# Kernel optimization log

Measured on AMD Instinct MI355X. Metric: run time of the kernel, lower is better.

The kernel has to match this reference:

```python
import jax, jax.numpy as jnp
import numpy as np

B, C, H, W = 8, 256, 64, 64


def setup_inputs() -> dict:
    key = jax.random.key(0)
    ks = jax.random.split(key, 9)
    s = 1.0 / np.sqrt(C)  # conv2d default init scale
    return {
        "foreground": jax.random.normal(ks[0], (B, C, H, W), jnp.float32),
        "background": jax.random.normal(ks[1], (B, C, H, W), jnp.float32),
        "mask": jax.random.uniform(ks[2], (B, C, H, W), jnp.float32),
        "Wq": jax.random.normal(ks[3], (C, C), jnp.float32) * s,
        "bq": jnp.zeros((C,), jnp.float32),
        "Wk": jax.random.normal(ks[4], (C, C), jnp.float32) * s,
        "bk": jnp.zeros((C,), jnp.float32),
        "Wv": jax.random.normal(ks[5], (C, C), jnp.float32) * s,
        "bv": jnp.zeros((C,), jnp.float32),
        "gamma": jnp.ones((1,), jnp.float32),
    }


def _conv1x1(x, Wt, b):
    # 1x1 conv == per-pixel channel matmul; x: [B,C,H,W], Wt: [Cout,Cin]
    return jnp.einsum('bchw,oc->bohw', x, Wt) + b[None, :, None, None]


def reference(foreground, background, mask, Wq, bq, Wk, bk, Wv, bv, gamma):
    b, c, h, w = foreground.shape
    hw = h * w
    # mask is already at feature resolution (interpolate would be identity)
    q = _conv1x1(foreground, Wq, bq).reshape(b, c, hw)   # [B,C,HW]
    k = _conv1x1(background, Wk, bk).reshape(b, c, hw)   # [B,C,HW]
    # bmm(q, k^T): channel-channel correlation [B,C,C]
    corr = jnp.einsum('bci,bdi->bcd', q, k)
    m_r = mask.reshape(b, c, hw)                          # [B,C,HW]
    # bmm(corr, m_r): mask-modulated scores [B,C,HW]
    scores = jnp.einsum('bcd,bdi->bci', corr, m_r)
    energy = jax.nn.softmax(scores, axis=-1)
    v = _conv1x1(foreground, Wv, bv).reshape(b, c, hw)
    attended = (energy * v).reshape(b, c, h, w)
    out = foreground * mask + gamma[0] * (1.0 - mask) * attended
    return out
```

## Files before the change

### kernel.cpp

```cpp
#include <hip/hip_runtime.h>
#include <math.h>

#define B_    8
#define C_    256
#define HW_   4096
#define CHW_  ((long)C_ * HW_)

#define BKT   32
#define LDH   40
#define KS    16
#define KCH   (HW_ / KS)

typedef __attribute__((ext_vector_type(8))) short bf16x8;
typedef __attribute__((ext_vector_type(4))) float f32x4;
#define MFMA_BF16(a, b, c) __builtin_amdgcn_mfma_f32_16x16x32_bf16((a), (b), (c), 0, 0, 0)

__device__ __forceinline__ void cvt_hl4(const float4 f, uint* h, uint* l) {
    uint u0 = __float_as_uint(f.x), u1 = __float_as_uint(f.y),
         u2 = __float_as_uint(f.z), u3 = __float_as_uint(f.w);
    uint h0 = (u0 + 0x8000u) & 0xFFFF0000u, h1 = (u1 + 0x8000u) & 0xFFFF0000u,
         h2 = (u2 + 0x8000u) & 0xFFFF0000u, h3 = (u3 + 0x8000u) & 0xFFFF0000u;
    h[0] = (h0 >> 16) | h1;
    h[1] = (h2 >> 16) | h3;
    float l0 = f.x - __uint_as_float(h0), l1 = f.y - __uint_as_float(h1),
          l2 = f.z - __uint_as_float(h2), l3 = f.w - __uint_as_float(h3);
    uint a0 = __float_as_uint(l0) & 0xFFFF0000u, a1 = __float_as_uint(l1) & 0xFFFF0000u,
         a2 = __float_as_uint(l2) & 0xFFFF0000u, a3 = __float_as_uint(l3) & 0xFFFF0000u;
    l[0] = (a0 >> 16) | a1;
    l[1] = (a2 >> 16) | a3;
}
__device__ __forceinline__ void cvt_h4(const float4 f, uint* h) {
    uint u0 = __float_as_uint(f.x), u1 = __float_as_uint(f.y),
         u2 = __float_as_uint(f.z), u3 = __float_as_uint(f.w);
    uint h0 = (u0 + 0x8000u) & 0xFFFF0000u, h1 = (u1 + 0x8000u) & 0xFFFF0000u,
         h2 = (u2 + 0x8000u) & 0xFFFF0000u, h3 = (u3 + 0x8000u) & 0xFFFF0000u;
    h[0] = (h0 >> 16) | h1;
    h[1] = (h2 >> 16) | h3;
}

__global__ __launch_bounds__(256, 2) void gemm_nt_mfma(
    const float* __restrict__ F, const float* __restrict__ G,
    float* __restrict__ part)
{
    __shared__ ushort Ah[128 * LDH], Al[128 * LDH], Bh[128 * LDH], Bl[128 * LDH];

    const int z  = blockIdx.z;
    const int b  = z >> 4;
    const int ks = z & (KS - 1);
    const int c0 = blockIdx.y * 128;
    const int d0 = blockIdx.x * 128;
    const float* Fb = F + (long)b * CHW_ + (long)ks * KCH;
    const float* Gb = G + (long)b * CHW_ + (long)ks * KCH;

    const int t    = threadIdx.x;
    const int srow = t >> 1;
    const int sk   = (t & 1) * 16;
    const int lane = t & 63, w = t >> 6;
    const int col  = lane & 15, quad = lane >> 4;
    const int wm   = (w >> 1) * 64, wn = (w & 1) * 64;

    f32x4 acc[4][4] = {};

    for (int kt = 0; kt < KCH; kt += BKT) {
        {
            const float* s = &Fb[(long)(c0 + srow) * HW_ + kt + sk];
            uint h[4], l[4];
            cvt_hl4(*reinterpret_cast<const float4*>(s),     h + 0, l + 0);
            cvt_hl4(*reinterpret_cast<const float4*>(s + 4), h + 2, l + 2);
            *reinterpret_cast<uint4*>(&Ah[srow * LDH + sk]) = make_uint4(h[0], h[1], h[2], h[3]);
            *reinterpret_cast<uint4*>(&Al[srow * LDH + sk]) = make_uint4(l[0], l[1], l[2], l[3]);
            cvt_hl4(*reinterpret_cast<const float4*>(s + 8),  h + 0, l + 0);
            cvt_hl4(*reinterpret_cast<const float4*>(s + 12), h + 2, l + 2);
            *reinterpret_cast<uint4*>(&Ah[srow * LDH + sk + 8]) = make_uint4(h[0], h[1], h[2], h[3]);
            *reinterpret_cast<uint4*>(&Al[srow * LDH + sk + 8]) = make_uint4(l[0], l[1], l[2], l[3]);
        }
        {
            const float* s = &Gb[(long)(d0 + srow) * HW_ + kt + sk];
            uint h[4], l[4];
            cvt_hl4(*reinterpret_cast<const float4*>(s),     h + 0, l + 0);
            cvt_hl4(*reinterpret_cast<const float4*>(s + 4), h + 2, l + 2);
            *reinterpret_cast<uint4*>(&Bh[srow * LDH + sk]) = make_uint4(h[0], h[1], h[2], h[3]);
            *reinterpret_cast<uint4*>(&Bl[srow * LDH + sk]) = make_uint4(l[0], l[1], l[2], l[3]);
            cvt_hl4(*reinterpret_cast<const float4*>(s + 8),  h + 0, l + 0);
            cvt_hl4(*reinterpret_cast<const float4*>(s + 12), h + 2, l + 2);
            *reinterpret_cast<uint4*>(&Bh[srow * LDH + sk + 8]) = make_uint4(h[0], h[1], h[2], h[3]);
            *reinterpret_cast<uint4*>(&Bl[srow * LDH + sk + 8]) = make_uint4(l[0], l[1], l[2], l[3]);
        }
        __syncthreads();

        bf16x8 bfh[4], bfl[4];
        #pragma unroll
        for (int tj = 0; tj < 4; ++tj) {
            const int r = (wn + tj * 16 + col) * LDH + quad * 8;
            bfh[tj] = *reinterpret_cast<const bf16x8*>(&Bh[r]);
            bfl[tj] = *reinterpret_cast<const bf16x8*>(&Bl[r]);
        }
        #pragma unroll
        for (int ti = 0; ti < 4; ++ti) {
            const int r = (wm + ti * 16 + col) * LDH + quad * 8;
            bf16x8 afh = *reinterpret_cast<const bf16x8*>(&Ah[r]);
            bf16x8 afl = *reinterpret_cast<const bf16x8*>(&Al[r]);
            #pragma unroll
            for (int tj = 0; tj < 4; ++tj) {
                acc[ti][tj] = MFMA_BF16(afh, bfh[tj], acc[ti][tj]);
                acc[ti][tj] = MFMA_BF16(afh, bfl[tj], acc[ti][tj]);
                acc[ti][tj] = MFMA_BF16(afl, bfh[tj], acc[ti][tj]);
            }
        }
        __syncthreads();
    }

    float* P = part + (long)z * C_ * C_;
    #pragma unroll
    for (int ti = 0; ti < 4; ++ti) {
        const int m = c0 + wm + ti * 16 + quad * 4;
        #pragma unroll
        for (int tj = 0; tj < 4; ++tj) {
            const int n = d0 + wn + tj * 16 + col;
            #pragma unroll
            for (int r = 0; r < 4; ++r)
                P[(long)(m + r) * C_ + n] = acc[ti][tj][r];
        }
    }
}

__global__ __launch_bounds__(256, 2) void gemm_scores_mfma(
    const float* __restrict__ corr,
    const ushort* __restrict__ mTh, const ushort* __restrict__ mTl,
    float* __restrict__ S)
{
    __shared__ ushort Ah[128 * LDH], Al[128 * LDH], Bh[128 * LDH], Bl[128 * LDH];

    const int b  = blockIdx.z;
    const int m0 = blockIdx.y * 128;
    const int n0 = blockIdx.x * 128;
    const float*  Ab  = corr + (long)b * C_ * C_;
    const ushort* Bhb = mTh + (long)b * CHW_;
    const ushort* Blb = mTl + (long)b * CHW_;

    const int t    = threadIdx.x;
    const int srow = t >> 1;
    const int sk   = (t & 1) * 16;
    const int lane = t & 63, w = t >> 6;
    const int col  = lane & 15, quad = lane >> 4;
    const int wm   = (w >> 1) * 64, wn = (w & 1) * 64;

    f32x4 acc[4][4] = {};

    for (int kt = 0; kt < C_; kt += BKT) {
        {
            const float* s = &Ab[(long)(m0 + srow) * C_ + kt + sk];
            uint h[4], l[4];
            cvt_hl4(*reinterpret_cast<const float4*>(s),     h + 0, l + 0);
            cvt_hl4(*reinterpret_cast<const float4*>(s + 4), h + 2, l + 2);
            *reinterpret_cast<uint4*>(&Ah[srow * LDH + sk]) = make_uint4(h[0], h[1], h[2], h[3]);
            *reinterpret_cast<uint4*>(&Al[srow * LDH + sk]) = make_uint4(l[0], l[1], l[2], l[3]);
            cvt_hl4(*reinterpret_cast<const float4*>(s + 8),  h + 0, l + 0);
            cvt_hl4(*reinterpret_cast<const float4*>(s + 12), h + 2, l + 2);
            *reinterpret_cast<uint4*>(&Ah[srow * LDH + sk + 8]) = make_uint4(h[0], h[1], h[2], h[3]);
            *reinterpret_cast<uint4*>(&Al[srow * LDH + sk + 8]) = make_uint4(l[0], l[1], l[2], l[3]);
        }
        {
            const long o = (long)(n0 + srow) * C_ + kt + sk;
            uint4 v0 = *reinterpret_cast<const uint4*>(&Bhb[o]);
            uint4 v1 = *reinterpret_cast<const uint4*>(&Bhb[o + 8]);
            uint4 w0 = *reinterpret_cast<const uint4*>(&Blb[o]);
            uint4 w1 = *reinterpret_cast<const uint4*>(&Blb[o + 8]);
            *reinterpret_cast<uint4*>(&Bh[srow * LDH + sk])     = v0;
            *reinterpret_cast<uint4*>(&Bh[srow * LDH + sk + 8]) = v1;
            *reinterpret_cast<uint4*>(&Bl[srow * LDH + sk])     = w0;
            *reinterpret_cast<uint4*>(&Bl[srow * LDH + sk + 8]) = w1;
        }
        __syncthreads();

        bf16x8 bfh[4], bfl[4];
        #pragma unroll
        for (int tj = 0; tj < 4; ++tj) {
            const int r = (wn + tj * 16 + col) * LDH + quad * 8;
            bfh[tj] = *reinterpret_cast<const bf16x8*>(&Bh[r]);
            bfl[tj] = *reinterpret_cast<const bf16x8*>(&Bl[r]);
        }
        #pragma unroll
        for (int ti = 0; ti < 4; ++ti) {
            const int r = (wm + ti * 16 + col) * LDH + quad * 8;
            bf16x8 afh = *reinterpret_cast<const bf16x8*>(&Ah[r]);
            bf16x8 afl = *reinterpret_cast<const bf16x8*>(&Al[r]);
            #pragma unroll
            for (int tj = 0; tj < 4; ++tj) {
                acc[ti][tj] = MFMA_BF16(afh, bfh[tj], acc[ti][tj]);
                acc[ti][tj] = MFMA_BF16(afh, bfl[tj], acc[ti][tj]);
                acc[ti][tj] = MFMA_BF16(afl, bfh[tj], acc[ti][tj]);
            }
        }
        __syncthreads();
    }

    float* Sb = S + (long)b * CHW_;
    #pragma unroll
    for (int ti = 0; ti < 4; ++ti) {
        const int m = m0 + wm + ti * 16 + quad * 4;
        #pragma unroll
        for (int tj = 0; tj < 4; ++tj) {
            const int n = n0 + wn + tj * 16 + col;
            #pragma unroll
            for (int r = 0; r < 4; ++r)
                Sb[(long)(m + r) * HW_ + n] = acc[ti][tj][r];
        }
    }
}

__global__ __launch_bounds__(256, 2) void gemm_v_final_mfma(
    const float* __restrict__ Wv, const ushort* __restrict__ fTh,
    const float* __restrict__ bv, const float* __restrict__ fg,
    const float* __restrict__ mask, const float* __restrict__ S,
    const float* __restrict__ stats, const float* __restrict__ gamma,
    float* __restrict__ out)
{
    __shared__ ushort Ahh[128 * LDH], Bhh[128 * LDH];

    const int b  = blockIdx.z;
    const int m0 = blockIdx.y * 128;
    const int n0 = blockIdx.x * 128;
    const ushort* Bb = fTh + (long)b * CHW_;

    const int t    = threadIdx.x;
    const int srow = t >> 1;
    const int sk   = (t & 1) * 16;
    const int lane = t & 63, w = t >> 6;
    const int col  = lane & 15, quad = lane >> 4;
    const int wm   = (w >> 1) * 64, wn = (w & 1) * 64;

    f32x4 acc[4][4] = {};

    for (int kt = 0; kt < C_; kt += BKT) {
        {
            const float* s = &Wv[(long)(m0 + srow) * C_ + kt + sk];
            uint h[4];
            cvt_h4(*reinterpret_cast<const float4*>(s),     h + 0);
            cvt_h4(*reinterpret_cast<const float4*>(s + 4), h + 2);
            *reinterpret_cast<uint4*>(&Ahh[srow * LDH + sk]) = make_uint4(h[0], h[1], h[2], h[3]);
            cvt_h4(*reinterpret_cast<const float4*>(s + 8),  h + 0);
            cvt_h4(*reinterpret_cast<const float4*>(s + 12), h + 2);
            *reinterpret_cast<uint4*>(&Ahh[srow * LDH + sk + 8]) = make_uint4(h[0], h[1], h[2], h[3]);
        }
        {
            const long o = (long)(n0 + srow) * C_ + kt + sk;
            uint4 v0 = *reinterpret_cast<const uint4*>(&Bb[o]);
            uint4 v1 = *reinterpret_cast<const uint4*>(&Bb[o + 8]);
            *reinterpret_cast<uint4*>(&Bhh[srow * LDH + sk])     = v0;
            *reinterpret_cast<uint4*>(&Bhh[srow * LDH + sk + 8]) = v1;
        }
        __syncthreads();

        bf16x8 bfh[4];
        #pragma unroll
        for (int tj = 0; tj < 4; ++tj)
            bfh[tj] = *reinterpret_cast<const bf16x8*>(&Bhh[(wn + tj * 16 + col) * LDH + quad * 8]);
        #pragma unroll
        for (int ti = 0; ti < 4; ++ti) {
            bf16x8 afh = *reinterpret_cast<const bf16x8*>(&Ahh[(wm + ti * 16 + col) * LDH + quad * 8]);
            #pragma unroll
            for (int tj = 0; tj < 4; ++tj)
                acc[ti][tj] = MFMA_BF16(afh, bfh[tj], acc[ti][tj]);
        }
        __syncthreads();
    }

    const float g = gamma[0];
    #pragma unroll
    for (int ti = 0; ti < 4; ++ti) {
        const int m = m0 + wm + ti * 16 + quad * 4;
        #pragma unroll
        for (int r = 0; r < 4; ++r) {
            const int row  = b * C_ + m + r;
            const float mx  = stats[row];
            const float inv = 1.0f / stats[B_ * C_ + row];
            const float bvm = bv[m + r];
            #pragma unroll
            for (int tj = 0; tj < 4; ++tj) {
                const int n = n0 + wn + tj * 16 + col;
                const long e = (long)b * CHW_ + (long)(m + r) * HW_ + n;
                const float f  = fg[e];
                const float mk = mask[e];
                const float sv = S[e];
                const float vv = acc[ti][tj][r] + bvm;
                out[e] = f * mk + g * (1.0f - mk) * (__expf(sv - mx) * inv) * vv;
            }
        }
    }
}

__global__ __launch_bounds__(256) void conv_transpose(
    const float* __restrict__ mask, const float* __restrict__ fg,
    ushort* __restrict__ mTh, ushort* __restrict__ mTl, ushort* __restrict__ fTh)
{
    __shared__ float tile[64][65];
    const int zi = blockIdx.z;
    const bool domask = zi < B_;
    const int b = domask ? zi : zi - B_;
    const float* src = (domask ? mask : fg) + (long)b * CHW_;
    const int e0 = blockIdx.y * 64, i0 = blockIdx.x * 64;

    const int t  = threadIdx.x;
    const int tr = t >> 4, tc = (t & 15) * 4;

    #pragma unroll
    for (int j = 0; j < 4; ++j) {
        const int e = tr + j * 16;
        float4 v = *reinterpret_cast<const float4*>(&src[(long)(e0 + e) * HW_ + i0 + tc]);
        tile[e][tc + 0] = v.x; tile[e][tc + 1] = v.y;
        tile[e][tc + 2] = v.z; tile[e][tc + 3] = v.w;
    }
    __syncthreads();

    #pragma unroll
    for (int j = 0; j < 4; ++j) {
        const int i = tr + j * 16;
        float4 v = make_float4(tile[tc + 0][i], tile[tc + 1][i], tile[tc + 2][i], tile[tc + 3][i]);
        const long o = (long)b * CHW_ + (long)(i0 + i) * C_ + e0 + tc;
        if (domask) {
            uint h[2], l[2];
            cvt_hl4(v, h, l);
            *reinterpret_cast<uint2*>(&mTh[o]) = make_uint2(h[0], h[1]);
            *reinterpret_cast<uint2*>(&mTl[o]) = make_uint2(l[0], l[1]);
        } else {
            uint h[2];
            cvt_h4(v, h);
            *reinterpret_cast<uint2*>(&fTh[o]) = make_uint2(h[0], h[1]);
        }
    }
}

__global__ __launch_bounds__(256) void rowsums(
    const float* __restrict__ fg, const float* __restrict__ bg,
    float* __restrict__ fsum, float* __restrict__ gsum)
{
    const int row = blockIdx.x;
    const int t   = threadIdx.x;
    const float* fr = fg + (long)row * HW_;
    const float* gr = bg + (long)row * HW_;
    float sf = 0.0f, sg = 0.0f;
    #pragma unroll
    for (int j = 0; j < 4; ++j) {
        float4 a = *reinterpret_cast<const float4*>(&fr[(j * 256 + t) * 4]);
        float4 c = *reinterpret_cast<const float4*>(&gr[(j * 256 + t) * 4]);
        sf += a.x + a.y + a.z + a.w;
        sg += c.x + c.y + c.z + c.w;
    }
    #pragma unroll
    for (int o = 32; o > 0; o >>= 1) { sf += __shfl_xor(sf, o); sg += __shfl_xor(sg, o); }
    __shared__ float red[8];
    const int wid = t >> 6;
    if ((t & 63) == 0) { red[wid] = sf; red[4 + wid] = sg; }
    __syncthreads();
    if (t == 0) {
        fsum[row] = red[0] + red[1] + red[2] + red[3];
        gsum[row] = red[4] + red[5] + red[6] + red[7];
    }
}

__global__ __launch_bounds__(256) void reduce_part(
    const float* __restrict__ part, float* __restrict__ S1)
{
    const long idx = (long)blockIdx.x * 256 + threadIdx.x;
    const int  b   = (int)(idx >> 16);
    const long e   = idx & 65535;
    const float* p = part + ((long)b * KS) * 65536 + e;
    float s = 0.0f;
    #pragma unroll
    for (int ks = 0; ks < KS; ++ks) s += p[(long)ks * 65536];
    S1[idx] = s;
}

__global__ __launch_bounds__(256) void uvw_kernel(
    const float* __restrict__ Wq, const float* __restrict__ Wk,
    const float* __restrict__ bk,
    const float* __restrict__ fsum, const float* __restrict__ gsum,
    float* __restrict__ u, float* __restrict__ wh)
{
    const int g = blockIdx.x * 256 + threadIdx.x;
    if (g < 2048) {
        const int b = g >> 8, c = g & 255;
        const float* w = Wq + (long)c * C_;
        const float* s = fsum + b * C_;
        float acc = 0.0f;
        for (int e = 0; e < C_; ++e) acc = fmaf(w[e], s[e], acc);
        u[g] = acc;
    } else {
        const int g2 = g - 2048;
        const int b = g2 >> 8, d = g2 & 255;
        const float* w = Wk + (long)d * C_;
        const float* s = gsum + b * C_;
        float acc = 0.0f;
        for (int f = 0; f < C_; ++f) acc = fmaf(w[f], s[f], acc);
        wh[g2] = acc + (float)HW_ * bk[d];
    }
}

#define BK64 16
#define LDT64 68
__global__ __launch_bounds__(256) void gemm_nt64(
    const float* __restrict__ S1, const float* __restrict__ Wk,
    float* __restrict__ T)
{
    __shared__ float As[BK64][LDT64];
    __shared__ float Bs[BK64][LDT64];
    const int r0 = blockIdx.y * 64;
    const int d0 = blockIdx.x * 64;
    const int t   = threadIdx.x;
    const int tx  = t & 15, ty = t >> 4;
    const int tx4 = tx * 4, ty4 = ty * 4;
    const int am  = t >> 2, ak4 = (t & 3) * 4;

    float acc[4][4] = {};
    for (int k0 = 0; k0 < C_; k0 += BK64) {
        float4 av = *reinterpret_cast<const float4*>(&S1[(long)(r0 + am) * C_ + k0 + ak4]);
        float4 bw = *reinterpret_cast<const float4*>(&Wk[(long)(d0 + am) * C_ + k0 + ak4]);
        As[ak4+0][am]=av.x; As[ak4+1][am]=av.y; As[ak4+2][am]=av.z; As[ak4+3][am]=av.w;
        Bs[ak4+0][am]=bw.x; Bs[ak4+1][am]=bw.y; Bs[ak4+2][am]=bw.z; Bs[ak4+3][am]=bw.w;
        __syncthreads();
        #pragma unroll
        for (int kk = 0; kk < BK64; ++kk) {
            float4 a = *reinterpret_cast<const float4*>(&As[kk][ty4]);
            float4 x = *reinterpret_cast<const float4*>(&Bs[kk][tx4]);
            const float ar[4] = {a.x,a.y,a.z,a.w};
            const float xr[4] = {x.x,x.y,x.z,x.w};
            #pragma unroll
            for (int r = 0; r < 4; ++r)
                #pragma unroll
                for (int s = 0; s < 4; ++s)
                    acc[r][s] = fmaf(ar[r], xr[s], acc[r][s]);
        }
        __syncthreads();
    }
    #pragma unroll
    for (int r = 0; r < 4; ++r) {
        float4 o; o.x=acc[r][0]; o.y=acc[r][1]; o.z=acc[r][2]; o.w=acc[r][3];
        *reinterpret_cast<float4*>(&T[(long)(r0 + ty4 + r) * C_ + d0 + tx4]) = o;
    }
}

__global__ __launch_bounds__(256) void gemm_nn64_rank1(
    const float* __restrict__ Wq, const float* __restrict__ T,
    const float* __restrict__ u,  const float* __restrict__ bk,
    const float* __restrict__ bq, const float* __restrict__ wh,
    float* __restrict__ corr)
{
    __shared__ float As[BK64][LDT64];
    __shared__ float Bs[BK64][LDT64];
    const int b  = blockIdx.z;
    const int m0 = blockIdx.y * 64;
    const int n0 = blockIdx.x * 64;
    const float* Tb = T + (long)b * C_ * C_;

    const int t   = threadIdx.x;
    const int tx  = t & 15, ty = t >> 4;
    const int tx4 = tx * 4, ty4 = ty * 4;
    const int am  = t >> 2, ak4 = (t & 3) * 4;
    const int xk  = ty,     xn4 = tx4;

    float acc[4][4] = {};
    for (int k0 = 0; k0 < C_; k0 += BK64) {
        float4 av = *reinterpret_cast<const float4*>(&Wq[(long)(m0 + am) * C_ + k0 + ak4]);
        float4 xv = *reinterpret_cast<const float4*>(&Tb[(long)(k0 + xk) * C_ + n0 + xn4]);
        As[ak4+0][am]=av.x; As[ak4+1][am]=av.y; As[ak4+2][am]=av.z; As[ak4+3][am]=av.w;
        *reinterpret_cast<float4*>(&Bs[xk][xn4]) = xv;
        __syncthreads();
        #pragma unroll
        for (int kk = 0; kk < BK64; ++kk) {
            float4 a = *reinterpret_cast<const float4*>(&As[kk][ty4]);
            float4 x = *reinterpret_cast<const float4*>(&Bs[kk][tx4]);
            const float ar[4] = {a.x,a.y,a.z,a.w};
            const float xr[4] = {x.x,x.y,x.z,x.w};
            #pragma unroll
            for (int r = 0; r < 4; ++r)
                #pragma unroll
                for (int s = 0; s < 4; ++s)
                    acc[r][s] = fmaf(ar[r], xr[s], acc[r][s]);
        }
        __syncthreads();
    }

    float4 bkv = *reinterpret_cast<const float4*>(&bk[n0 + tx4]);
    float4 whv = *reinterpret_cast<const float4*>(&wh[b * C_ + n0 + tx4]);
    float* Yb = corr + (long)b * C_ * C_;
    #pragma unroll
    for (int r = 0; r < 4; ++r) {
        const int m = m0 + ty4 + r;
        const float um = u[b * C_ + m];
        const float bm = bq[m];
        float4 o;
        o.x = acc[r][0] + um*bkv.x + bm*whv.x;
        o.y = acc[r][1] + um*bkv.y + bm*whv.y;
        o.z = acc[r][2] + um*bkv.z + bm*whv.z;
        o.w = acc[r][3] + um*bkv.w + bm*whv.w;
        *reinterpret_cast<float4*>(&Yb[(long)m * C_ + n0 + tx4]) = o;
    }
}

__global__ __launch_bounds__(256) void softmax_stats(
    const float* __restrict__ S, float* __restrict__ stats)
{
    const int row = blockIdx.x;
    const float* sr = S + (long)row * HW_;
    const int t = threadIdx.x;
    float4 x[4];
    #pragma unroll
    for (int j = 0; j < 4; ++j)
        x[j] = *reinterpret_cast<const float4*>(&sr[(j * 256 + t) * 4]);
    float m = -INFINITY;
    #pragma unroll
    for (int j = 0; j < 4; ++j)
        m = fmaxf(m, fmaxf(fmaxf(x[j].x, x[j].y), fmaxf(x[j].z, x[j].w)));
    __shared__ float red[8];
    #pragma unroll
    for (int o = 32; o > 0; o >>= 1) m = fmaxf(m, __shfl_xor(m, o));
    const int wid = t >> 6;
    if ((t & 63) == 0) red[wid] = m;
    __syncthreads();
    m = fmaxf(fmaxf(red[0], red[1]), fmaxf(red[2], red[3]));
    float sum = 0.0f;
    #pragma unroll
    for (int j = 0; j < 4; ++j)
        sum += __expf(x[j].x - m) + __expf(x[j].y - m)
             + __expf(x[j].z - m) + __expf(x[j].w - m);
    #pragma unroll
    for (int o = 32; o > 0; o >>= 1) sum += __shfl_xor(sum, o);
    if ((t & 63) == 0) red[4 + wid] = sum;
    __syncthreads();
    if (t == 0) {
        stats[row]            = m;
        stats[B_ * C_ + row]  = red[4] + red[5] + red[6] + red[7];
    }
}

extern "C" void kernel_launch(void* const* d_in, const int* in_sizes, int n_in,
                              void* d_out, int out_size, void* d_ws, size_t ws_size,
                              hipStream_t stream)
{
    const float* fg    = (const float*)d_in[0];
    const float* bg    = (const float*)d_in[1];
    const float* mask  = (const float*)d_in[2];
    const float* Wq    = (const float*)d_in[3];
    const float* bq    = (const float*)d_in[4];
    const float* Wk    = (const float*)d_in[5];
    const float* bk    = (const float*)d_in[6];
    const float* Wv    = (const float*)d_in[7];
    const float* bv    = (const float*)d_in[8];
    const float* gamma = (const float*)d_in[9];
    float* out = (float*)d_out;

    char* ws = (char*)d_ws;
    float*  part   = (float*)(ws);
    float*  scores = (float*)(ws);
    ushort* mTh    = (ushort*)(ws + 33554432);
    ushort* mTl    = (ushort*)(ws + 50331648);
    ushort* fTh    = (ushort*)(ws + 67108864);
    float*  S1     = (float*)(ws + 83886080);
    float*  T      = (float*)(ws + 85983232);
    float*  corr   = (float*)(ws + 88080384);
    float*  stats  = (float*)(ws + 90177536);
    float*  fsum   = (float*)(ws + 90193920);
    float*  gsum   = (float*)(ws + 90202112);
    float*  u      = (float*)(ws + 90210304);
    float*  wh     = (float*)(ws + 90218496);

    const dim3 blk(256);

    rowsums<<<dim3(B_ * C_), blk, 0, stream>>>(fg, bg, fsum, gsum);

    conv_transpose<<<dim3(HW_ / 64, C_ / 64, 2 * B_), blk, 0, stream>>>(
        mask, fg, mTh, mTl, fTh);

    gemm_nt_mfma<<<dim3(2, 2, B_ * KS), blk, 0, stream>>>(fg, bg, part);
    reduce_part<<<dim3(B_ * C_ * C_ / 256), blk, 0, stream>>>(part, S1);

    uvw_kernel<<<dim3(16), blk, 0, stream>>>(Wq, Wk, bk, fsum, gsum, u, wh);

    gemm_nt64<<<dim3(C_ / 64, B_ * C_ / 64), blk, 0, stream>>>(S1, Wk, T);
    gemm_nn64_rank1<<<dim3(4, 4, B_), blk, 0, stream>>>(Wq, T, u, bk, bq, wh, corr);

    gemm_scores_mfma<<<dim3(HW_ / 128, C_ / 128, B_), blk, 0, stream>>>(
        corr, mTh, mTl, scores);

    softmax_stats<<<dim3(B_ * C_), blk, 0, stream>>>(scores, stats);

    gemm_v_final_mfma<<<dim3(HW_ / 128, C_ / 128, B_), blk, 0, stream>>>(
        Wv, fTh, bv, fg, mask, scores, stats, gamma, out);
}
```

Measured before the change: 293.5 us.

## Precompute bf16 hi/lo splits upstream so MFMA GEMMs load pre-converted operands

The fp32-to-bf16 hi/lo split is moved out of the GEMM inner loops. A new prep kernel converts foreground and background (fused with the row sums), a small kernel converts Wv, and the corr producer writes hi/lo halves directly. The GEMMs now copy ready-made bf16 tiles into LDS and use a launch-bounds occupancy hint of 3. This removes repeated per-tile conversion ALU work, since each tile is converted many times across blocks. In exchange it adds a full extra pass that writes and then re-reads 4 bf16 buffers of the 8x256x4096 inputs, plus a larger workspace.

```diff
diff --git a/kernel.cpp b/kernel.cpp
--- a/kernel.cpp
+++ b/kernel.cpp
@@ -38,256 +38,52 @@
     h[1] = (h2 >> 16) | h3;
 }
 
-__global__ __launch_bounds__(256, 2) void gemm_nt_mfma(
-    const float* __restrict__ F, const float* __restrict__ G,
-    float* __restrict__ part)
-{
-    __shared__ ushort Ah[128 * LDH], Al[128 * LDH], Bh[128 * LDH], Bl[128 * LDH];
-
-    const int z  = blockIdx.z;
-    const int b  = z >> 4;
-    const int ks = z & (KS - 1);
-    const int c0 = blockIdx.y * 128;
-    const int d0 = blockIdx.x * 128;
-    const float* Fb = F + (long)b * CHW_ + (long)ks * KCH;
-    const float* Gb = G + (long)b * CHW_ + (long)ks * KCH;
-
-    const int t    = threadIdx.x;
-    const int srow = t >> 1;
-    const int sk   = (t & 1) * 16;
-    const int lane = t & 63, w = t >> 6;
-    const int col  = lane & 15, quad = lane >> 4;
-    const int wm   = (w >> 1) * 64, wn = (w & 1) * 64;
-
-    f32x4 acc[4][4] = {};
-
-    for (int kt = 0; kt < KCH; kt += BKT) {
-        {
-            const float* s = &Fb[(long)(c0 + srow) * HW_ + kt + sk];
-            uint h[4], l[4];
-            cvt_hl4(*reinterpret_cast<const float4*>(s),     h + 0, l + 0);
-            cvt_hl4(*reinterpret_cast<const float4*>(s + 4), h + 2, l + 2);
-            *reinterpret_cast<uint4*>(&Ah[srow * LDH + sk]) = make_uint4(h[0], h[1], h[2], h[3]);
-            *reinterpret_cast<uint4*>(&Al[srow * LDH + sk]) = make_uint4(l[0], l[1], l[2], l[3]);
-            cvt_hl4(*reinterpret_cast<const float4*>(s + 8),  h + 0, l + 0);
-            cvt_hl4(*reinterpret_cast<const float4*>(s + 12), h + 2, l + 2);
-            *reinterpret_cast<uint4*>(&Ah[srow * LDH + sk + 8]) = make_uint4(h[0], h[1], h[2], h[3]);
-            *reinterpret_cast<uint4*>(&Al[srow * LDH + sk + 8]) = make_uint4(l[0], l[1], l[2], l[3]);
-        }
-        {
-            const float* s = &Gb[(long)(d0 + srow) * HW_ + kt + sk];
-            uint h[4], l[4];
-            cvt_hl4(*reinterpret_cast<const float4*>(s),     h + 0, l + 0);
-            cvt_hl4(*reinterpret_cast<const float4*>(s + 4), h + 2, l + 2);
-            *reinterpret_cast<uint4*>(&Bh[srow * LDH + sk]) = make_uint4(h[0], h[1], h[2], h[3]);
-            *reinterpret_cast<uint4*>(&Bl[srow * LDH + sk]) = make_uint4(l[0], l[1], l[2], l[3]);
-            cvt_hl4(*reinterpret_cast<const float4*>(s + 8),  h + 0, l + 0);
-            cvt_hl4(*reinterpret_cast<const float4*>(s + 12), h + 2, l + 2);
-            *reinterpret_cast<uint4*>(&Bh[srow * LDH + sk + 8]) = make_uint4(h[0], h[1], h[2], h[3]);
-            *reinterpret_cast<uint4*>(&Bl[srow * LDH + sk + 8]) = make_uint4(l[0], l[1], l[2], l[3]);
-        }
-        __syncthreads();
-
-        bf16x8 bfh[4], bfl[4];
-        #pragma unroll
-        for (int tj = 0; tj < 4; ++tj) {
-            const int r = (wn + tj * 16 + col) * LDH + quad * 8;
-            bfh[tj] = *reinterpret_cast<const bf16x8*>(&Bh[r]);
-            bfl[tj] = *reinterpret_cast<const bf16x8*>(&Bl[r]);
-        }
-        #pragma unroll
-        for (int ti = 0; ti < 4; ++ti) {
-            const int r = (wm + ti * 16 + col) * LDH + quad * 8;
-            bf16x8 afh = *reinterpret_cast<const bf16x8*>(&Ah[r]);
-            bf16x8 afl = *reinterpret_cast<const bf16x8*>(&Al[r]);
-            #pragma unroll
-            for (int tj = 0; tj < 4; ++tj) {
-                acc[ti][tj] = MFMA_BF16(afh, bfh[tj], acc[ti][tj]);
-                acc[ti][tj] = MFMA_BF16(afh, bfl[tj], acc[ti][tj]);
-                acc[ti][tj] = MFMA_BF16(afl, bfh[tj], acc[ti][tj]);
-            }
-        }
-        __syncthreads();
-    }
-
-    float* P = part + (long)z * C_ * C_;
-    #pragma unroll
-    for (int ti = 0; ti < 4; ++ti) {
-        const int m = c0 + wm + ti * 16 + quad * 4;
-        #pragma unroll
-        for (int tj = 0; tj < 4; ++tj) {
-            const int n = d0 + wn + tj * 16 + col;
-            #pragma unroll
-            for (int r = 0; r < 4; ++r)
-                P[(long)(m + r) * C_ + n] = acc[ti][tj][r];
-        }
-    }
-}
-
-__global__ __launch_bounds__(256, 2) void gemm_scores_mfma(
-    const float* __restrict__ corr,
-    const ushort* __restrict__ mTh, const ushort* __restrict__ mTl,
-    float* __restrict__ S)
-{
-    __shared__ ushort Ah[128 * LDH], Al[128 * LDH], Bh[128 * LDH], Bl[128 * LDH];
-
-    const int b  = blockIdx.z;
-    const int m0 = blockIdx.y * 128;
-    const int n0 = blockIdx.x * 128;
-    const float*  Ab  = corr + (long)b * C_ * C_;
-    const ushort* Bhb = mTh + (long)b * CHW_;
-    const ushort* Blb = mTl + (long)b * CHW_;
-
-    const int t    = threadIdx.x;
-    const int srow = t >> 1;
-    const int sk   = (t & 1) * 16;
-    const int lane = t & 63, w = t >> 6;
-    const int col  = lane & 15, quad = lane >> 4;
-    const int wm   = (w >> 1) * 64, wn = (w & 1) * 64;
-
-    f32x4 acc[4][4] = {};
-
-    for (int kt = 0; kt < C_; kt += BKT) {
-        {
-            const float* s = &Ab[(long)(m0 + srow) * C_ + kt + sk];
-            uint h[4], l[4];
-            cvt_hl4(*reinterpret_cast<const float4*>(s),     h + 0, l + 0);
-            cvt_hl4(*reinterpret_cast<const float4*>(s + 4), h + 2, l + 2);
-            *reinterpret_cast<uint4*>(&Ah[srow * LDH + sk]) = make_uint4(h[0], h[1], h[2], h[3]);
-            *reinterpret_cast<uint4*>(&Al[srow * LDH + sk]) = make_uint4(l[0], l[1], l[2], l[3]);
-            cvt_hl4(*reinterpret_cast<const float4*>(s + 8),  h + 0, l + 0);
-            cvt_hl4(*reinterpret_cast<const float4*>(s + 12), h + 2, l + 2);
-            *reinterpret_cast<uint4*>(&Ah[srow * LDH + sk + 8]) = make_uint4(h[0], h[1], h[2], h[3]);
-            *reinterpret_cast<uint4*>(&Al[srow * LDH + sk + 8]) = make_uint4(l[0], l[1], l[2], l[3]);
-        }
-        {
-            const long o = (long)(n0 + srow) * C_ + kt + sk;
-            uint4 v0 = *reinterpret_cast<const uint4*>(&Bhb[o]);
-            uint4 v1 = *reinterpret_cast<const uint4*>(&Bhb[o + 8]);
-            uint4 w0 = *reinterpret_cast<const uint4*>(&Blb[o]);
-            uint4 w1 = *reinterpret_cast<const uint4*>(&Blb[o + 8]);
-            *reinterpret_cast<uint4*>(&Bh[srow * LDH + sk])     = v0;
-            *reinterpret_cast<uint4*>(&Bh[srow * LDH + sk + 8]) = v1;
-            *reinterpret_cast<uint4*>(&Bl[srow * LDH + sk])     = w0;
-            *reinterpret_cast<uint4*>(&Bl[srow * LDH + sk + 8]) = w1;
-        }
-        __syncthreads();
-
-        bf16x8 bfh[4], bfl[4];
-        #pragma unroll
-        for (int tj = 0; tj < 4; ++tj) {
-            const int r = (wn + tj * 16 + col) * LDH + quad * 8;
-            bfh[tj] = *reinterpret_cast<const bf16x8*>(&Bh[r]);
-            bfl[tj] = *reinterpret_cast<const bf16x8*>(&Bl[r]);
-        }
-        #pragma unroll
-        for (int ti = 0; ti < 4; ++ti) {
-            const int r = (wm + ti * 16 + col) * LDH + quad * 8;
-            bf16x8 afh = *reinterpret_cast<const bf16x8*>(&Ah[r]);
-            bf16x8 afl = *reinterpret_cast<const bf16x8*>(&Al[r]);
-            #pragma unroll
-            for (int tj = 0; tj < 4; ++tj) {
-                acc[ti][tj] = MFMA_BF16(afh, bfh[tj], acc[ti][tj]);
-                acc[ti][tj] = MFMA_BF16(afh, bfl[tj], acc[ti][tj]);
-                acc[ti][tj] = MFMA_BF16(afl, bfh[tj], acc[ti][tj]);
-            }
-        }
-        __syncthreads();
-    }
-
-    float* Sb = S + (long)b * CHW_;
-    #pragma unroll
-    for (int ti = 0; ti < 4; ++ti) {
-        const int m = m0 + wm + ti * 16 + quad * 4;
-        #pragma unroll
-        for (int tj = 0; tj < 4; ++tj) {
-            const int n = n0 + wn + tj * 16 + col;
-            #pragma unroll
-            for (int r = 0; r < 4; ++r)
-                Sb[(long)(m + r) * HW_ + n] = acc[ti][tj][r];
-        }
-    }
-}
-
-__global__ __launch_bounds__(256, 2) void gemm_v_final_mfma(
-    const float* __restrict__ Wv, const ushort* __restrict__ fTh,
-    const float* __restrict__ bv, const float* __restrict__ fg,
-    const float* __restrict__ mask, const float* __restrict__ S,
-    const float* __restrict__ stats, const float* __restrict__ gamma,
-    float* __restrict__ out)
-{
-    __shared__ ushort Ahh[128 * LDH], Bhh[128 * LDH];
-
-    const int b  = blockIdx.z;
-    const int m0 = blockIdx.y * 128;
-    const int n0 = blockIdx.x * 128;
-    const ushort* Bb = fTh + (long)b * CHW_;
-
-    const int t    = threadIdx.x;
-    const int srow = t >> 1;
-    const int sk   = (t & 1) * 16;
-    const int lane = t & 63, w = t >> 6;
-    const int col  = lane & 15, quad = lane >> 4;
-    const int wm   = (w >> 1) * 64, wn = (w & 1) * 64;
-
-    f32x4 acc[4][4] = {};
-
-    for (int kt = 0; kt < C_; kt += BKT) {
-        {
-            const float* s = &Wv[(long)(m0 + srow) * C_ + kt + sk];
-            uint h[4];
-            cvt_h4(*reinterpret_cast<const float4*>(s),     h + 0);
-            cvt_h4(*reinterpret_cast<const float4*>(s + 4), h + 2);
-            *reinterpret_cast<uint4*>(&Ahh[srow * LDH + sk]) = make_uint4(h[0], h[1], h[2], h[3]);
-            cvt_h4(*reinterpret_cast<const float4*>(s + 8),  h + 0);
-            cvt_h4(*reinterpret_cast<const float4*>(s + 12), h + 2);
-            *reinterpret_cast<uint4*>(&Ahh[srow * LDH + sk + 8]) = make_uint4(h[0], h[1], h[2], h[3]);
-        }
-        {
-            const long o = (long)(n0 + srow) * C_ + kt + sk;
-            uint4 v0 = *reinterpret_cast<const uint4*>(&Bb[o]);
-            uint4 v1 = *reinterpret_cast<const uint4*>(&Bb[o + 8]);
-            *reinterpret_cast<uint4*>(&Bhh[srow * LDH + sk])     = v0;
-            *reinterpret_cast<uint4*>(&Bhh[srow * LDH + sk + 8]) = v1;
-        }
-        __syncthreads();
-
-        bf16x8 bfh[4];
-        #pragma unroll
-        for (int tj = 0; tj < 4; ++tj)
-            bfh[tj] = *reinterpret_cast<const bf16x8*>(&Bhh[(wn + tj * 16 + col) * LDH + quad * 8]);
-        #pragma unroll
-        for (int ti = 0; ti < 4; ++ti) {
-            bf16x8 afh = *reinterpret_cast<const bf16x8*>(&Ahh[(wm + ti * 16 + col) * LDH + quad * 8]);
-            #pragma unroll
-            for (int tj = 0; tj < 4; ++tj)
-                acc[ti][tj] = MFMA_BF16(afh, bfh[tj], acc[ti][tj]);
-        }
-        __syncthreads();
-    }
-
-    const float g = gamma[0];
-    #pragma unroll
-    for (int ti = 0; ti < 4; ++ti) {
-        const int m = m0 + wm + ti * 16 + quad * 4;
-        #pragma unroll
-        for (int r = 0; r < 4; ++r) {
-            const int row  = b * C_ + m + r;
-            const float mx  = stats[row];
-            const float inv = 1.0f / stats[B_ * C_ + row];
-            const float bvm = bv[m + r];
-            #pragma unroll
-            for (int tj = 0; tj < 4; ++tj) {
-                const int n = n0 + wn + tj * 16 + col;
-                const long e = (long)b * CHW_ + (long)(m + r) * HW_ + n;
-                const float f  = fg[e];
-                const float mk = mask[e];
-                const float sv = S[e];
-                const float vv = acc[ti][tj][r] + bvm;
-                out[e] = f * mk + g * (1.0f - mk) * (__expf(sv - mx) * inv) * vv;
-            }
-        }
-    }
+__global__ __launch_bounds__(256) void prep_hl(
+    const float* __restrict__ fg, const float* __restrict__ bg,
+    ushort* __restrict__ fgh, ushort* __restrict__ fgl,
+    ushort* __restrict__ bgh, ushort* __restrict__ bgl,
+    float* __restrict__ fsum, float* __restrict__ gsum)
+{
+    const int row = blockIdx.x;
+    const int t   = threadIdx.x;
+    const long base = (long)row * HW_;
+
+    float sf = 0.0f, sg = 0.0f;
+    #pragma unroll
+    for (int j = 0; j < 4; ++j) {
+        const int idx = (j * 256 + t) * 4;
+        float4 a = *reinterpret_cast<const float4*>(&fg[base + idx]);
+        float4 c = *reinterpret_cast<const float4*>(&bg[base + idx]);
+        uint h[2], l[2];
+        cvt_hl4(a, h, l);
+        *reinterpret_cast<uint2*>(&fgh[base + idx]) = make_uint2(h[0], h[1]);
+        *reinterpret_cast<uint2*>(&fgl[base + idx]) = make_uint2(l[0], l[1]);
+        cvt_hl4(c, h, l);
+        *reinterpret_cast<uint2*>(&bgh[base + idx]) = make_uint2(h[0], h[1]);
+        *reinterpret_cast<uint2*>(&bgl[base + idx]) = make_uint2(l[0], l[1]);
+        sf += a.x + a.y + a.z + a.w;
+        sg += c.x + c.y + c.z + c.w;
+    }
+    #pragma unroll
+    for (int o = 32; o > 0; o >>= 1) { sf += __shfl_xor(sf, o); sg += __shfl_xor(sg, o); }
+    __shared__ float red[8];
+    const int wid = t >> 6;
+    if ((t & 63) == 0) { red[wid] = sf; red[4 + wid] = sg; }
+    __syncthreads();
+    if (t == 0) {
+        fsum[row] = red[0] + red[1] + red[2] + red[3];
+        gsum[row] = red[4] + red[5] + red[6] + red[7];
+    }
+}
+
+__global__ __launch_bounds__(256) void conv_w(
+    const float* __restrict__ Wv, ushort* __restrict__ Wvh)
+{
+    const int i = (blockIdx.x * 256 + threadIdx.x) * 4;
+    float4 v = *reinterpret_cast<const float4*>(&Wv[i]);
+    uint h[2];
+    cvt_h4(v, h);
+    *reinterpret_cast<uint2*>(&Wvh[i]) = make_uint2(h[0], h[1]);
 }
 
 __global__ __launch_bounds__(256) void conv_transpose(
@@ -331,31 +127,238 @@
     }
 }
 
-__global__ __launch_bounds__(256) void rowsums(
-    const float* __restrict__ fg, const float* __restrict__ bg,
-    float* __restrict__ fsum, float* __restrict__ gsum)
-{
-    const int row = blockIdx.x;
-    const int t   = threadIdx.x;
-    const float* fr = fg + (long)row * HW_;
-    const float* gr = bg + (long)row * HW_;
-    float sf = 0.0f, sg = 0.0f;
-    #pragma unroll
-    for (int j = 0; j < 4; ++j) {
-        float4 a = *reinterpret_cast<const float4*>(&fr[(j * 256 + t) * 4]);
-        float4 c = *reinterpret_cast<const float4*>(&gr[(j * 256 + t) * 4]);
-        sf += a.x + a.y + a.z + a.w;
-        sg += c.x + c.y + c.z + c.w;
-    }
-    #pragma unroll
-    for (int o = 32; o > 0; o >>= 1) { sf += __shfl_xor(sf, o); sg += __shfl_xor(sg, o); }
-    __shared__ float red[8];
-    const int wid = t >> 6;
-    if ((t & 63) == 0) { red[wid] = sf; red[4 + wid] = sg; }
-    __syncthreads();
-    if (t == 0) {
-        fsum[row] = red[0] + red[1] + red[2] + red[3];
-        gsum[row] = red[4] + red[5] + red[6] + red[7];
+__global__ __launch_bounds__(256, 3) void gemm_nt_mfma(
+    const ushort* __restrict__ Fh, const ushort* __restrict__ Fl,
+    const ushort* __restrict__ Gh, const ushort* __restrict__ Gl,
+    float* __restrict__ part)
+{
+    __shared__ ushort Ah[128 * LDH], Al[128 * LDH], Bh[128 * LDH], Bl[128 * LDH];
+
+    const int z  = blockIdx.z;
+    const int b  = z >> 4;
+    const int ks = z & (KS - 1);
+    const int c0 = blockIdx.y * 128;
+    const int d0 = blockIdx.x * 128;
+    const long boff = (long)b * CHW_ + (long)ks * KCH;
+
+    const int t    = threadIdx.x;
+    const int srow = t >> 1;
+    const int sk   = (t & 1) * 16;
+    const int lane = t & 63, w = t >> 6;
+    const int col  = lane & 15, quad = lane >> 4;
+    const int wm   = (w >> 1) * 64, wn = (w & 1) * 64;
+
+    f32x4 acc[4][4] = {};
+
+    for (int kt = 0; kt < KCH; kt += BKT) {
+        const long ga = boff + (long)(c0 + srow) * HW_ + kt + sk;
+        const long gb = boff + (long)(d0 + srow) * HW_ + kt + sk;
+        uint4 ah0 = *reinterpret_cast<const uint4*>(&Fh[ga]);
+        uint4 ah1 = *reinterpret_cast<const uint4*>(&Fh[ga + 8]);
+        uint4 al0 = *reinterpret_cast<const uint4*>(&Fl[ga]);
+        uint4 al1 = *reinterpret_cast<const uint4*>(&Fl[ga + 8]);
+        uint4 bh0 = *reinterpret_cast<const uint4*>(&Gh[gb]);
+        uint4 bh1 = *reinterpret_cast<const uint4*>(&Gh[gb + 8]);
+        uint4 bl0 = *reinterpret_cast<const uint4*>(&Gl[gb]);
+        uint4 bl1 = *reinterpret_cast<const uint4*>(&Gl[gb + 8]);
+        *reinterpret_cast<uint4*>(&Ah[srow * LDH + sk])     = ah0;
+        *reinterpret_cast<uint4*>(&Ah[srow * LDH + sk + 8]) = ah1;
+        *reinterpret_cast<uint4*>(&Al[srow * LDH + sk])     = al0;
+        *reinterpret_cast<uint4*>(&Al[srow * LDH + sk + 8]) = al1;
+        *reinterpret_cast<uint4*>(&Bh[srow * LDH + sk])     = bh0;
+        *reinterpret_cast<uint4*>(&Bh[srow * LDH + sk + 8]) = bh1;
+        *reinterpret_cast<uint4*>(&Bl[srow * LDH + sk])     = bl0;
+        *reinterpret_cast<uint4*>(&Bl[srow * LDH + sk + 8]) = bl1;
+        __syncthreads();
+
+        bf16x8 bfh[4], bfl[4];
+        #pragma unroll
+        for (int tj = 0; tj < 4; ++tj) {
+            const int r = (wn + tj * 16 + col) * LDH + quad * 8;
+            bfh[tj] = *reinterpret_cast<const bf16x8*>(&Bh[r]);
+            bfl[tj] = *reinterpret_cast<const bf16x8*>(&Bl[r]);
+        }
+        #pragma unroll
+        for (int ti = 0; ti < 4; ++ti) {
+            const int r = (wm + ti * 16 + col) * LDH + quad * 8;
+            bf16x8 afh = *reinterpret_cast<const bf16x8*>(&Ah[r]);
+            bf16x8 afl = *reinterpret_cast<const bf16x8*>(&Al[r]);
+            #pragma unroll
+            for (int tj = 0; tj < 4; ++tj) {
+                acc[ti][tj] = MFMA_BF16(afh, bfh[tj], acc[ti][tj]);
+                acc[ti][tj] = MFMA_BF16(afh, bfl[tj], acc[ti][tj]);
+                acc[ti][tj] = MFMA_BF16(afl, bfh[tj], acc[ti][tj]);
+            }
+        }
+        __syncthreads();
+    }
+
+    float* P = part + (long)z * C_ * C_;
+    #pragma unroll
+    for (int ti = 0; ti < 4; ++ti) {
+        const int m = c0 + wm + ti * 16 + quad * 4;
+        #pragma unroll
+        for (int tj = 0; tj < 4; ++tj) {
+            const int n = d0 + wn + tj * 16 + col;
+            #pragma unroll
+            for (int r = 0; r < 4; ++r)
+                P[(long)(m + r) * C_ + n] = acc[ti][tj][r];
+        }
+    }
+}
+
+__global__ __launch_bounds__(256, 3) void gemm_scores_mfma(
+    const ushort* __restrict__ corrh, const ushort* __restrict__ corrl,
+    const ushort* __restrict__ mTh,   const ushort* __restrict__ mTl,
+    float* __restrict__ S)
+{
+    __shared__ ushort Ah[128 * LDH], Al[128 * LDH], Bh[128 * LDH], Bl[128 * LDH];
+
+    const int b  = blockIdx.z;
+    const int m0 = blockIdx.y * 128;
+    const int n0 = blockIdx.x * 128;
+    const ushort* Ahb = corrh + (long)b * C_ * C_;
+    const ushort* Alb = corrl + (long)b * C_ * C_;
+    const ushort* Bhb = mTh + (long)b * CHW_;
+    const ushort* Blb = mTl + (long)b * CHW_;
+
+    const int t    = threadIdx.x;
+    const int srow = t >> 1;
+    const int sk   = (t & 1) * 16;
+    const int lane = t & 63, w = t >> 6;
+    const int col  = lane & 15, quad = lane >> 4;
+    const int wm   = (w >> 1) * 64, wn = (w & 1) * 64;
+
+    f32x4 acc[4][4] = {};
+
+    for (int kt = 0; kt < C_; kt += BKT) {
+        const long ga = (long)(m0 + srow) * C_ + kt + sk;
+        const long gb = (long)(n0 + srow) * C_ + kt + sk;
+        uint4 ah0 = *reinterpret_cast<const uint4*>(&Ahb[ga]);
+        uint4 ah1 = *reinterpret_cast<const uint4*>(&Ahb[ga + 8]);
+        uint4 al0 = *reinterpret_cast<const uint4*>(&Alb[ga]);
+        uint4 al1 = *reinterpret_cast<const uint4*>(&Alb[ga + 8]);
+        uint4 bh0 = *reinterpret_cast<const uint4*>(&Bhb[gb]);
+        uint4 bh1 = *reinterpret_cast<const uint4*>(&Bhb[gb + 8]);
+        uint4 bl0 = *reinterpret_cast<const uint4*>(&Blb[gb]);
+        uint4 bl1 = *reinterpret_cast<const uint4*>(&Blb[gb + 8]);
+        *reinterpret_cast<uint4*>(&Ah[srow * LDH + sk])     = ah0;
+        *reinterpret_cast<uint4*>(&Ah[srow * LDH + sk + 8]) = ah1;
+        *reinterpret_cast<uint4*>(&Al[srow * LDH + sk])     = al0;
+        *reinterpret_cast<uint4*>(&Al[srow * LDH + sk + 8]) = al1;
+        *reinterpret_cast<uint4*>(&Bh[srow * LDH + sk])     = bh0;
+        *reinterpret_cast<uint4*>(&Bh[srow * LDH + sk + 8]) = bh1;
+        *reinterpret_cast<uint4*>(&Bl[srow * LDH + sk])     = bl0;
+        *reinterpret_cast<uint4*>(&Bl[srow * LDH + sk + 8]) = bl1;
+        __syncthreads();
+
+        bf16x8 bfh[4], bfl[4];
+        #pragma unroll
+        for (int tj = 0; tj < 4; ++tj) {
+            const int r = (wn + tj * 16 + col) * LDH + quad * 8;
+            bfh[tj] = *reinterpret_cast<const bf16x8*>(&Bh[r]);
+            bfl[tj] = *reinterpret_cast<const bf16x8*>(&Bl[r]);
+        }
+        #pragma unroll
+        for (int ti = 0; ti < 4; ++ti) {
+            const int r = (wm + ti * 16 + col) * LDH + quad * 8;
+            bf16x8 afh = *reinterpret_cast<const bf16x8*>(&Ah[r]);
+            bf16x8 afl = *reinterpret_cast<const bf16x8*>(&Al[r]);
+            #pragma unroll
+            for (int tj = 0; tj < 4; ++tj) {
+                acc[ti][tj] = MFMA_BF16(afh, bfh[tj], acc[ti][tj]);
+                acc[ti][tj] = MFMA_BF16(afh, bfl[tj], acc[ti][tj]);
+                acc[ti][tj] = MFMA_BF16(afl, bfh[tj], acc[ti][tj]);
+            }
+        }
+        __syncthreads();
+    }
+
+    float* Sb = S + (long)b * CHW_;
+    #pragma unroll
+    for (int ti = 0; ti < 4; ++ti) {
+        const int m = m0 + wm + ti * 16 + quad * 4;
+        #pragma unroll
+        for (int tj = 0; tj < 4; ++tj) {
+            const int n = n0 + wn + tj * 16 + col;
+            #pragma unroll
+            for (int r = 0; r < 4; ++r)
+                Sb[(long)(m + r) * HW_ + n] = acc[ti][tj][r];
+        }
+    }
+}
+
+__global__ __launch_bounds__(256, 3) void gemm_v_final_mfma(
+    const ushort* __restrict__ Wvh, const ushort* __restrict__ fTh,
+    const float* __restrict__ bv, const float* __restrict__ fg,
+    const float* __restrict__ mask, const float* __restrict__ S,
+    const float* __restrict__ stats, const float* __restrict__ gamma,
+    float* __restrict__ out)
+{
+    __shared__ ushort Ahh[128 * LDH], Bhh[128 * LDH];
+
+    const int b  = blockIdx.z;
+    const int m0 = blockIdx.y * 128;
+    const int n0 = blockIdx.x * 128;
+    const ushort* Bb = fTh + (long)b * CHW_;
+
+    const int t    = threadIdx.x;
+    const int srow = t >> 1;
+    const int sk   = (t & 1) * 16;
+    const int lane = t & 63, w = t >> 6;
+    const int col  = lane & 15, quad = lane >> 4;
+    const int wm   = (w >> 1) * 64, wn = (w & 1) * 64;
+
+    f32x4 acc[4][4] = {};
+
+    for (int kt = 0; kt < C_; kt += BKT) {
+        const long ga = (long)(m0 + srow) * C_ + kt + sk;
+        const long gb = (long)(n0 + srow) * C_ + kt + sk;
+        uint4 a0 = *reinterpret_cast<const uint4*>(&Wvh[ga]);
+        uint4 a1 = *reinterpret_cast<const uint4*>(&Wvh[ga + 8]);
+        uint4 b0 = *reinterpret_cast<const uint4*>(&Bb[gb]);
+        uint4 b1 = *reinterpret_cast<const uint4*>(&Bb[gb + 8]);
+        *reinterpret_cast<uint4*>(&Ahh[srow * LDH + sk])     = a0;
+        *reinterpret_cast<uint4*>(&Ahh[srow * LDH + sk + 8]) = a1;
+        *reinterpret_cast<uint4*>(&Bhh[srow * LDH + sk])     = b0;
+        *reinterpret_cast<uint4*>(&Bhh[srow * LDH + sk + 8]) = b1;
+        __syncthreads();
+
+        bf16x8 bfh[4];
+        #pragma unroll
+        for (int tj = 0; tj < 4; ++tj)
+            bfh[tj] = *reinterpret_cast<const bf16x8*>(&Bhh[(wn + tj * 16 + col) * LDH + quad * 8]);
+        #pragma unroll
+        for (int ti = 0; ti < 4; ++ti) {
+            bf16x8 afh = *reinterpret_cast<const bf16x8*>(&Ahh[(wm + ti * 16 + col) * LDH + quad * 8]);
+            #pragma unroll
+            for (int tj = 0; tj < 4; ++tj)
+                acc[ti][tj] = MFMA_BF16(afh, bfh[tj], acc[ti][tj]);
+        }
+        __syncthreads();
+    }
+
+    const float g = gamma[0];
+    #pragma unroll
+    for (int ti = 0; ti < 4; ++ti) {
+        const int m = m0 + wm + ti * 16 + quad * 4;
+        #pragma unroll
+        for (int r = 0; r < 4; ++r) {
+            const int row  = b * C_ + m + r;
+            const float mx  = stats[row];
+            const float inv = 1.0f / stats[B_ * C_ + row];
+            const float bvm = bv[m + r];
+            #pragma unroll
+            for (int tj = 0; tj < 4; ++tj) {
+                const int n = n0 + wn + tj * 16 + col;
+                const long e = (long)b * CHW_ + (long)(m + r) * HW_ + n;
+                const float f  = fg[e];
+                const float mk = mask[e];
+                const float sv = S[e];
+                const float vv = acc[ti][tj][r] + bvm;
+                out[e] = f * mk + g * (1.0f - mk) * (__expf(sv - mx) * inv) * vv;
+            }
+        }
     }
 }
 
@@ -444,7 +447,7 @@
     const float* __restrict__ Wq, const float* __restrict__ T,
     const float* __restrict__ u,  const float* __restrict__ bk,
     const float* __restrict__ bq, const float* __restrict__ wh,
-    float* __restrict__ corr)
+    ushort* __restrict__ corrh, ushort* __restrict__ corrl)
 {
     __shared__ float As[BK64][LDT64];
     __shared__ float Bs[BK64][LDT64];
@@ -483,7 +486,6 @@
 
     float4 bkv = *reinterpret_cast<const float4*>(&bk[n0 + tx4]);
     float4 whv = *reinterpret_cast<const float4*>(&wh[b * C_ + n0 + tx4]);
-    float* Yb = corr + (long)b * C_ * C_;
     #pragma unroll
     for (int r = 0; r < 4; ++r) {
         const int m = m0 + ty4 + r;
@@ -494,7 +496,11 @@
         o.y = acc[r][1] + um*bkv.y + bm*whv.y;
         o.z = acc[r][2] + um*bkv.z + bm*whv.z;
         o.w = acc[r][3] + um*bkv.w + bm*whv.w;
-        *reinterpret_cast<float4*>(&Yb[(long)m * C_ + n0 + tx4]) = o;
+        uint h[2], l[2];
+        cvt_hl4(o, h, l);
+        const long e = (long)b * C_ * C_ + (long)m * C_ + n0 + tx4;
+        *reinterpret_cast<uint2*>(&corrh[e]) = make_uint2(h[0], h[1]);
+        *reinterpret_cast<uint2*>(&corrl[e]) = make_uint2(l[0], l[1]);
     }
 }
 
@@ -553,38 +559,45 @@
     char* ws = (char*)d_ws;
     float*  part   = (float*)(ws);
     float*  scores = (float*)(ws);
-    ushort* mTh    = (ushort*)(ws + 33554432);
-    ushort* mTl    = (ushort*)(ws + 50331648);
-    ushort* fTh    = (ushort*)(ws + 67108864);
-    float*  S1     = (float*)(ws + 83886080);
-    float*  T      = (float*)(ws + 85983232);
-    float*  corr   = (float*)(ws + 88080384);
-    float*  stats  = (float*)(ws + 90177536);
-    float*  fsum   = (float*)(ws + 90193920);
-    float*  gsum   = (float*)(ws + 90202112);
-    float*  u      = (float*)(ws + 90210304);
-    float*  wh     = (float*)(ws + 90218496);
+    ushort* fgh    = (ushort*)(ws + 33554432);
+    ushort* fgl    = (ushort*)(ws + 50331648);
+    ushort* bgh    = (ushort*)(ws + 67108864);
+    ushort* bgl    = (ushort*)(ws + 83886080);
+    ushort* mTh    = (ushort*)(ws + 100663296);
+    ushort* mTl    = (ushort*)(ws + 117440512);
+    ushort* fTh    = (ushort*)(ws + 134217728);
+    float*  S1     = (float*)(ws + 150994944);
+    float*  T      = (float*)(ws + 153092096);
+    ushort* corrh  = (ushort*)(ws + 155189248);
+    ushort* corrl  = (ushort*)(ws + 156237824);
+    ushort* Wvh    = (ushort*)(ws + 157286400);
+    float*  stats  = (float*)(ws + 157417472);
+    float*  fsum   = (float*)(ws + 157433856);
+    float*  gsum   = (float*)(ws + 157442048);
+    float*  u      = (float*)(ws + 157450240);
+    float*  wh     = (float*)(ws + 157458432);
 
     const dim3 blk(256);
 
-    rowsums<<<dim3(B_ * C_), blk, 0, stream>>>(fg, bg, fsum, gsum);
+    prep_hl<<<dim3(B_ * C_), blk, 0, stream>>>(fg, bg, fgh, fgl, bgh, bgl, fsum, gsum);
 
     conv_transpose<<<dim3(HW_ / 64, C_ / 64, 2 * B_), blk, 0, stream>>>(
         mask, fg, mTh, mTl, fTh);
-
-    gemm_nt_mfma<<<dim3(2, 2, B_ * KS), blk, 0, stream>>>(fg, bg, part);
+    conv_w<<<dim3(64), blk, 0, stream>>>(Wv, Wvh);
+
+    gemm_nt_mfma<<<dim3(2, 2, B_ * KS), blk, 0, stream>>>(fgh, fgl, bgh, bgl, part);
     reduce_part<<<dim3(B_ * C_ * C_ / 256), blk, 0, stream>>>(part, S1);
 
     uvw_kernel<<<dim3(16), blk, 0, stream>>>(Wq, Wk, bk, fsum, gsum, u, wh);
 
     gemm_nt64<<<dim3(C_ / 64, B_ * C_ / 64), blk, 0, stream>>>(S1, Wk, T);
-    gemm_nn64_rank1<<<dim3(4, 4, B_), blk, 0, stream>>>(Wq, T, u, bk, bq, wh, corr);
+    gemm_nn64_rank1<<<dim3(4, 4, B_), blk, 0, stream>>>(Wq, T, u, bk, bq, wh, corrh, corrl);
 
     gemm_scores_mfma<<<dim3(HW_ / 128, C_ / 128, B_), blk, 0, stream>>>(
-        corr, mTh, mTl, scores);
+        corrh, corrl, mTh, mTl, scores);
 
     softmax_stats<<<dim3(B_ * C_), blk, 0, stream>>>(scores, stats);
 
     gemm_v_final_mfma<<<dim3(HW_ / 128, C_ / 128, B_), blk, 0, stream>>>(
-        Wv, fTh, bv, fg, mask, scores, stats, gamma, out);
-}
+        Wvh, fTh, bv, fg, mask, scores, stats, gamma, out);
+}
```

Result: slower. 317.3 us (+8.1%).
